# Optimization experiments

Hardware: AMD Instinct MI355X
Metric: run time of the kernel (lower is better)

Reference implementation:

```python
import jax, jax.numpy as jnp
import numpy as np

IN_FEATURES = 4096
OUT_FEATURES = 11008
GROUP_SIZE = 128


def setup_inputs() -> dict:
    key = jax.random.key(0)
    k_x, k_w, k_s, k_z, k_b = jax.random.split(key, 5)
    x = jax.random.normal(k_x, (8, IN_FEATURES), dtype=jnp.float32)
    # packed INT4 weights: two 4-bit values per byte, stored in int32 (0..255)
    weight_q = jax.random.randint(k_w, (OUT_FEATURES, IN_FEATURES // 2), 0, 256, dtype=jnp.int32)
    num_groups = IN_FEATURES // GROUP_SIZE  # 32
    scales = jax.random.uniform(k_s, (OUT_FEATURES, num_groups), dtype=jnp.float32) * 0.01 + 1e-4
    zeros = jax.random.normal(k_z, (OUT_FEATURES, num_groups), dtype=jnp.float32) * 0.05
    bias = jax.random.normal(k_b, (OUT_FEATURES,), dtype=jnp.float32) * 0.02
    return {"x": x, "weight_q": weight_q, "scales": scales, "zeros": zeros, "bias": bias}


def _dequantize(weight_q, scales, zeros):
    # unpack INT4: low nibble first, then high nibble (matches torch stack order)
    low = weight_q & 15
    high = (weight_q >> 4) & 15
    q = jnp.stack([low, high], axis=-1).reshape(OUT_FEATURES, -1)  # [out, in]
    q = q.astype(scales.dtype)
    num_groups = scales.shape[1]
    q = q[:, : num_groups * GROUP_SIZE].reshape(OUT_FEATURES, num_groups, GROUP_SIZE)
    w = q * scales[:, :, None] + zeros[:, :, None]
    return w.reshape(OUT_FEATURES, -1)[:, :IN_FEATURES]


def reference(x, weight_q, scales, zeros, bias):
    w = _dequantize(weight_q, scales, zeros)            # [out, in]
    return x.astype(w.dtype) @ w.T + bias               # [B, out]
```

## Files before the change

### kernel.cpp

```cpp
#include <hip/hip_runtime.h>

typedef _Float16 f16;
typedef __attribute__((ext_vector_type(2))) _Float16 f16x2;
typedef __attribute__((ext_vector_type(4))) _Float16 f16x4;
typedef __attribute__((ext_vector_type(8))) _Float16 f16x8;
typedef __attribute__((ext_vector_type(4))) float f32x4;
typedef __attribute__((ext_vector_type(4))) unsigned u32x4;

constexpr int IN_F  = 4096;
constexpr int OUT_F = 11008;
constexpr int NGRP  = 32;
constexpr int NTILE = OUT_F / 16;
constexpr int PLANE = OUT_F * 8;

__device__ __forceinline__ unsigned dq2(unsigned q, f16x2 sp, f16x2 zp) {
    unsigned t = (((q << 12) | q) & 0x000F000Fu) | 0x64006400u;
    f16x2 u = __builtin_bit_cast(f16x2, t);
    u = u - (f16x2){(_Float16)1024.0f, (_Float16)1024.0f};
    u = u * sp + zp;
    return __builtin_bit_cast(unsigned, u);
}

__device__ __forceinline__ f16x2 bcast(float v) {
    _Float16 h = (_Float16)v;
    return (f16x2){h, h};
}

__global__ void xprep_kernel(const float* __restrict__ x, f16* __restrict__ xh) {
    int i = (blockIdx.x * blockDim.x + threadIdx.x) * 4;
    float4 v = *(const float4*)(x + i);
    f16x4 r = {(f16)v.x, (f16)v.y, (f16)v.z, (f16)v.w};
    *(f16x4*)(xh + i) = r;
}

__global__ __launch_bounds__(256, 4)
void qlin_pipe(const int* __restrict__ wq,
               const float* __restrict__ scales,
               const float* __restrict__ zeros,
               const f16* __restrict__ xh,
               float* __restrict__ wsf)
{
    __shared__ unsigned char wlds[4][2][2048];

    const int tid  = threadIdx.x;
    const int wv   = tid >> 6;
    const int lane = tid & 63;
    const int col  = lane & 15;
    const int kg   = lane >> 4;
    const int bid  = blockIdx.x;
    const int kq   = bid & 3;
    const int ot   = bid >> 2;
    const int o0   = ot * 16;
    const int orow = o0 + col;
    const int k0   = kq * 1024 + wv * 256;
    const int g0   = k0 >> 7;
    const bool mvalid = (col < 8);

    float2 sg = *(const float2*)(scales + (size_t)orow * NGRP + g0);
    float2 zg = *(const float2*)(zeros  + (size_t)orow * NGRP + g0);

    f16x8 af[4][2];
    const f16* xcol = xh + (size_t)col * IN_F + k0 + kg * 8;
    #pragma unroll
    for (int ss = 0; ss < 4; ++ss) {
        if (mvalid) {
            af[ss][0] = *(const f16x8*)(xcol + ss * 64);
            af[ss][1] = *(const f16x8*)(xcol + ss * 64 + 32);
        } else {
            af[ss][0] = (f16x8){0,0,0,0,0,0,0,0};
            af[ss][1] = (f16x8){0,0,0,0,0,0,0,0};
        }
    }

    const char* wb   = (const char*)wq;
    const int   coff = (lane & 7) * 16;

    auto stageW = [&](int ss) {
        const int b = ss & 1;
        #pragma unroll
        for (int j = 0; j < 2; ++j) {
            const int r = j * 8 + (lane >> 3);
            const char* src = wb + (size_t)(o0 + r) * 8192
                              + (size_t)(k0 + ss * 64) * 2
                              + (coff ^ ((r & 7) << 4));
            __builtin_amdgcn_global_load_lds(
                (const __attribute__((address_space(1))) void*)src,
                (__attribute__((address_space(3))) void*)&wlds[wv][b][j * 1024],
                16, 0, 0);
        }
    };

    stageW(0); __builtin_amdgcn_sched_barrier(0);
    stageW(1); __builtin_amdgcn_sched_barrier(0);

    const unsigned rswz = (unsigned)((col & 7) << 4);
    f32x4 acc = {0.f, 0.f, 0.f, 0.f};

    #pragma unroll
    for (int ss = 0; ss < 4; ++ss) {
        if (ss < 3) asm volatile("s_waitcnt vmcnt(2)" ::: "memory");
        else        asm volatile("s_waitcnt vmcnt(0)" ::: "memory");
        __builtin_amdgcn_sched_barrier(0);

        const unsigned char* buf = &wlds[wv][ss & 1][0];
        const int4 qa = *(const int4*)(buf + (col * 128 + ((     kg * 16) ^ rswz)));
        const int4 qb = *(const int4*)(buf + (col * 128 + ((64 + kg * 16) ^ rswz)));

        asm volatile("s_waitcnt lgkmcnt(0)" ::: "memory");
        __builtin_amdgcn_sched_barrier(0);
        if (ss < 2) { stageW(ss + 2); __builtin_amdgcn_sched_barrier(0); }

        const f16x2 s2 = bcast((ss < 2) ? sg.x : sg.y);
        const f16x2 z2 = bcast((ss < 2) ? zg.x : zg.y);
        u32x4 ba = {dq2((unsigned)qa.x, s2, z2), dq2((unsigned)qa.y, s2, z2),
                    dq2((unsigned)qa.z, s2, z2), dq2((unsigned)qa.w, s2, z2)};
        u32x4 bb = {dq2((unsigned)qb.x, s2, z2), dq2((unsigned)qb.y, s2, z2),
                    dq2((unsigned)qb.z, s2, z2), dq2((unsigned)qb.w, s2, z2)};
        acc = __builtin_amdgcn_mfma_f32_16x16x32_f16(af[ss][0],
                __builtin_bit_cast(f16x8, ba), acc, 0, 0, 0);
        acc = __builtin_amdgcn_mfma_f32_16x16x32_f16(af[ss][1],
                __builtin_bit_cast(f16x8, bb), acc, 0, 0, 0);
    }

    *(f32x4*)&wlds[wv][0][lane * 16] = acc;
    __syncthreads();

    if (tid < 32) {
        f32x4 ssum = *(const f32x4*)&wlds[0][0][tid * 16];
        #pragma unroll
        for (int w = 1; w < 4; ++w)
            ssum += *(const f32x4*)&wlds[w][0][tid * 16];
        const int n = tid & 15;
        const int mbase = (tid >> 4) * 4;
        float* plane = wsf + (size_t)kq * PLANE;
        #pragma unroll
        for (int i = 0; i < 4; ++i)
            plane[(size_t)(mbase + i) * OUT_F + o0 + n] = ssum[i];
    }
}

__global__ __launch_bounds__(256)
void reduce_kernel(const float* __restrict__ wsf,
                   const float* __restrict__ bias,
                   float* __restrict__ out)
{
    const int idx = blockIdx.x * 256 + threadIdx.x;
    const int o = idx % OUT_F;
    out[idx] = bias[o] + wsf[idx] + wsf[PLANE + idx]
             + wsf[2 * PLANE + idx] + wsf[3 * PLANE + idx];
}

__global__ __launch_bounds__(256, 4)
void qlin_kernel(const int* __restrict__ wq,
                 const float* __restrict__ scales,
                 const float* __restrict__ zeros,
                 const float* __restrict__ bias,
                 const float* __restrict__ xf,
                 float* __restrict__ out)
{
    __shared__ unsigned char wlds[2][16][1024];
    __shared__ f32x4 red[4][64];

    const int tid  = threadIdx.x;
    const int wv   = tid >> 6;
    const int lane = tid & 63;
    const int col  = lane & 15;
    const int kg   = lane >> 4;
    const int o0   = blockIdx.x * 16;
    const int orow = o0 + col;
    const bool mvalid = (col < 8);

    f16x2 sp[8], zp[8];
    #pragma unroll
    for (int s = 0; s < 8; ++s) {
        sp[s] = bcast(scales[(size_t)orow * NGRP + s * 4 + wv]);
        zp[s] = bcast(zeros [(size_t)orow * NGRP + s * 4 + wv]);
    }

    const char* wtile = (const char*)wq + (size_t)o0 * 8192;
    auto stage = [&](int sl, int bufi) {
        #pragma unroll
        for (int c = 0; c < 4; ++c) {
            const int r = 4 * wv + c;
            const char* src = wtile + (size_t)r * 8192 + sl * 1024
                              + ((lane * 16) ^ ((r & 7) << 4));
            __builtin_amdgcn_global_load_lds(
                (const __attribute__((address_space(1))) void*)src,
                (__attribute__((address_space(3))) void*)&wlds[bufi][r][0],
                16, 0, 0);
        }
    };

    stage(0, 0);
    stage(1, 1);

    const float* xfcol = xf + (size_t)col * IN_F;
    const unsigned swz = (unsigned)((col & 7) << 4);
    f32x4 acc = {0.f, 0.f, 0.f, 0.f};

    #pragma unroll
    for (int s = 0; s < 8; ++s) {
        asm volatile("s_waitcnt vmcnt(0)" ::: "memory");
        __builtin_amdgcn_s_barrier();
        asm volatile("" ::: "memory");

        const f16x2 s2 = sp[s], z2 = zp[s];
        #pragma unroll
        for (int t = 0; t < 4; ++t) {
            const int k = s * 512 + wv * 128 + t * 32 + kg * 8;
            f16x8 af = (f16x8){0,0,0,0,0,0,0,0};
            if (mvalid) {
                float4 a0 = *(const float4*)(xfcol + k);
                float4 a1 = *(const float4*)(xfcol + k + 4);
                af = (f16x8){(f16)a0.x,(f16)a0.y,(f16)a0.z,(f16)a0.w,
                             (f16)a1.x,(f16)a1.y,(f16)a1.z,(f16)a1.w};
            }
            const unsigned off = ((unsigned)(wv * 256 + t * 64 + kg * 16)) ^ swz;
            const int4 q = *(const int4*)&wlds[s & 1][col][off];
            u32x4 bw = {dq2((unsigned)q.x, s2, z2),
                        dq2((unsigned)q.y, s2, z2),
                        dq2((unsigned)q.z, s2, z2),
                        dq2((unsigned)q.w, s2, z2)};
            f16x8 bfr = __builtin_bit_cast(f16x8, bw);
            acc = __builtin_amdgcn_mfma_f32_16x16x32_f16(af, bfr, acc, 0, 0, 0);
        }

        asm volatile("" ::: "memory");
        __builtin_amdgcn_s_barrier();
        if (s < 6) stage(s + 2, s & 1);
    }

    red[wv][lane] = acc;
    __syncthreads();

    if (tid < 64) {
        f32x4 ssum = red[0][tid];
        #pragma unroll
        for (int w = 1; w < 4; ++w) ssum += red[w][tid];
        const int n = tid & 15;
        const float bb = bias[o0 + n];
        const int mbase = (tid >> 4) * 4;
        if (mbase < 8) {
            #pragma unroll
            for (int i = 0; i < 4; ++i)
                out[(size_t)(mbase + i) * OUT_F + o0 + n] = ssum[i] + bb;
        }
    }
}

extern "C" void kernel_launch(void* const* d_in, const int* in_sizes, int n_in,
                              void* d_out, int out_size, void* d_ws, size_t ws_size,
                              hipStream_t stream) {
    const float* x  = (const float*)d_in[0];
    const int*   wq = (const int*)d_in[1];
    const float* sc = (const float*)d_in[2];
    const float* zr = (const float*)d_in[3];
    const float* bs = (const float*)d_in[4];
    float* out = (float*)d_out;
    (void)in_sizes; (void)n_in;

    const size_t planes_b = (size_t)4 * PLANE * sizeof(float);
    const size_t xh_b     = (size_t)8 * IN_F * sizeof(f16);

    if (ws_size >= planes_b + xh_b) {
        float* wsf = (float*)d_ws;
        f16*   xh  = (f16*)((char*)d_ws + planes_b);
        xprep_kernel<<<(8 * IN_F) / (256 * 4), 256, 0, stream>>>(x, xh);
        qlin_pipe<<<NTILE * 4, 256, 0, stream>>>(wq, sc, zr, xh, wsf);
        reduce_kernel<<<PLANE / 256, 256, 0, stream>>>(wsf, bs, out);
    } else {
        qlin_kernel<<<NTILE, 256, 0, stream>>>(wq, sc, zr, bs, x, out);
    }
}
```

Measured before the change: 28.80 us.

## Issue all weight LDS loads up front and zero-pad x to sixteen rows

The double-buffered two-stage weight pipeline becomes a single burst: all four 2KB stages per wave are issued into a larger 8KB-per-wave LDS buffer, with staged vmcnt waits as each stage is consumed. The activation prep kernel now writes a zero-padded 16-row fp16 copy of x, so the main kernel loads A fragments unconditionally and interleaves them with the weight loads. This removes the mid-loop LDS waits and the reissue of stages, and drops the per-lane validity branch. In exchange LDS use per block grows from 16KB to 32KB, which can cap resident blocks per CU, and the prep kernel writes twice as much.

```diff
diff --git a/kernel.cpp b/kernel.cpp
--- a/kernel.cpp
+++ b/kernel.cpp
@@ -26,21 +26,29 @@
     return (f16x2){h, h};
 }
 
-__global__ void xprep_kernel(const float* __restrict__ x, f16* __restrict__ xh) {
-    int i = (blockIdx.x * blockDim.x + threadIdx.x) * 4;
-    float4 v = *(const float4*)(x + i);
-    f16x4 r = {(f16)v.x, (f16)v.y, (f16)v.z, (f16)v.w};
-    *(f16x4*)(xh + i) = r;
+__global__ void xprep16_kernel(const float* __restrict__ x, f16* __restrict__ xh) {
+    const int i4  = blockIdx.x * blockDim.x + threadIdx.x;
+    const int k4  = i4 * 4;
+    const int row = k4 >> 12;
+    const int kk  = k4 & 4095;
+    f16x4 r;
+    if (row < 8) {
+        float4 v = *(const float4*)(x + (size_t)row * IN_F + kk);
+        r = (f16x4){(f16)v.x, (f16)v.y, (f16)v.z, (f16)v.w};
+    } else {
+        r = (f16x4){0, 0, 0, 0};
+    }
+    *(f16x4*)(xh + (size_t)row * IN_F + kk) = r;
 }
 
 __global__ __launch_bounds__(256, 4)
-void qlin_pipe(const int* __restrict__ wq,
-               const float* __restrict__ scales,
-               const float* __restrict__ zeros,
-               const f16* __restrict__ xh,
-               float* __restrict__ wsf)
+void qlin_burst(const int* __restrict__ wq,
+                const float* __restrict__ scales,
+                const float* __restrict__ zeros,
+                const f16* __restrict__ xh,
+                float* __restrict__ wsf)
 {
-    __shared__ unsigned char wlds[4][2][2048];
+    __shared__ unsigned char wlds[4][8192];
 
     const int tid  = threadIdx.x;
     const int wv   = tid >> 6;
@@ -54,29 +62,19 @@
     const int orow = o0 + col;
     const int k0   = kq * 1024 + wv * 256;
     const int g0   = k0 >> 7;
-    const bool mvalid = (col < 8);
 
     float2 sg = *(const float2*)(scales + (size_t)orow * NGRP + g0);
     float2 zg = *(const float2*)(zeros  + (size_t)orow * NGRP + g0);
-
-    f16x8 af[4][2];
-    const f16* xcol = xh + (size_t)col * IN_F + k0 + kg * 8;
-    #pragma unroll
-    for (int ss = 0; ss < 4; ++ss) {
-        if (mvalid) {
-            af[ss][0] = *(const f16x8*)(xcol + ss * 64);
-            af[ss][1] = *(const f16x8*)(xcol + ss * 64 + 32);
-        } else {
-            af[ss][0] = (f16x8){0,0,0,0,0,0,0,0};
-            af[ss][1] = (f16x8){0,0,0,0,0,0,0,0};
-        }
-    }
+    __builtin_amdgcn_sched_barrier(0);
 
     const char* wb   = (const char*)wq;
     const int   coff = (lane & 7) * 16;
-
-    auto stageW = [&](int ss) {
-        const int b = ss & 1;
+    const f16*  xcol = xh + (size_t)col * IN_F + k0 + kg * 8;
+
+    f16x8 af[4][2];
+
+    #pragma unroll
+    for (int ss = 0; ss < 4; ++ss) {
         #pragma unroll
         for (int j = 0; j < 2; ++j) {
             const int r = j * 8 + (lane >> 3);
@@ -85,30 +83,30 @@
                               + (coff ^ ((r & 7) << 4));
             __builtin_amdgcn_global_load_lds(
                 (const __attribute__((address_space(1))) void*)src,
-                (__attribute__((address_space(3))) void*)&wlds[wv][b][j * 1024],
+                (__attribute__((address_space(3))) void*)&wlds[wv][ss * 2048 + j * 1024],
                 16, 0, 0);
         }
-    };
-
-    stageW(0); __builtin_amdgcn_sched_barrier(0);
-    stageW(1); __builtin_amdgcn_sched_barrier(0);
-
-    const unsigned rswz = (unsigned)((col & 7) << 4);
+        af[ss][0] = *(const f16x8*)(xcol + ss * 64);
+        af[ss][1] = *(const f16x8*)(xcol + ss * 64 + 32);
+        __builtin_amdgcn_sched_barrier(0);
+    }
+
+    const unsigned rswz  = (unsigned)((col & 7) << 4);
+    const unsigned rbase = (unsigned)((col >> 3) * 1024 + (col & 7) * 128);
+
     f32x4 acc = {0.f, 0.f, 0.f, 0.f};
 
     #pragma unroll
     for (int ss = 0; ss < 4; ++ss) {
-        if (ss < 3) asm volatile("s_waitcnt vmcnt(2)" ::: "memory");
-        else        asm volatile("s_waitcnt vmcnt(0)" ::: "memory");
+        if      (ss == 0) asm volatile("s_waitcnt vmcnt(12)" ::: "memory");
+        else if (ss == 1) asm volatile("s_waitcnt vmcnt(8)"  ::: "memory");
+        else if (ss == 2) asm volatile("s_waitcnt vmcnt(4)"  ::: "memory");
+        else              asm volatile("s_waitcnt vmcnt(0)"  ::: "memory");
         __builtin_amdgcn_sched_barrier(0);
 
-        const unsigned char* buf = &wlds[wv][ss & 1][0];
-        const int4 qa = *(const int4*)(buf + (col * 128 + ((     kg * 16) ^ rswz)));
-        const int4 qb = *(const int4*)(buf + (col * 128 + ((64 + kg * 16) ^ rswz)));
-
-        asm volatile("s_waitcnt lgkmcnt(0)" ::: "memory");
-        __builtin_amdgcn_sched_barrier(0);
-        if (ss < 2) { stageW(ss + 2); __builtin_amdgcn_sched_barrier(0); }
+        const unsigned char* buf = &wlds[wv][ss * 2048];
+        const int4 qa = *(const int4*)(buf + rbase + ((     kg * 16) ^ rswz));
+        const int4 qb = *(const int4*)(buf + rbase + ((64 + kg * 16) ^ rswz));
 
         const f16x2 s2 = bcast((ss < 2) ? sg.x : sg.y);
         const f16x2 z2 = bcast((ss < 2) ? zg.x : zg.y);
@@ -122,14 +120,14 @@
                 __builtin_bit_cast(f16x8, bb), acc, 0, 0, 0);
     }
 
-    *(f32x4*)&wlds[wv][0][lane * 16] = acc;
+    *(f32x4*)&wlds[wv][lane * 16] = acc;
     __syncthreads();
 
     if (tid < 32) {
-        f32x4 ssum = *(const f32x4*)&wlds[0][0][tid * 16];
+        f32x4 ssum = *(const f32x4*)&wlds[0][tid * 16];
         #pragma unroll
         for (int w = 1; w < 4; ++w)
-            ssum += *(const f32x4*)&wlds[w][0][tid * 16];
+            ssum += *(const f32x4*)&wlds[w][tid * 16];
         const int n = tid & 15;
         const int mbase = (tid >> 4) * 4;
         float* plane = wsf + (size_t)kq * PLANE;
@@ -260,13 +258,13 @@
     (void)in_sizes; (void)n_in;
 
     const size_t planes_b = (size_t)4 * PLANE * sizeof(float);
-    const size_t xh_b     = (size_t)8 * IN_F * sizeof(f16);
+    const size_t xh_b     = (size_t)16 * IN_F * sizeof(f16);
 
     if (ws_size >= planes_b + xh_b) {
         float* wsf = (float*)d_ws;
         f16*   xh  = (f16*)((char*)d_ws + planes_b);
-        xprep_kernel<<<(8 * IN_F) / (256 * 4), 256, 0, stream>>>(x, xh);
-        qlin_pipe<<<NTILE * 4, 256, 0, stream>>>(wq, sc, zr, xh, wsf);
+        xprep16_kernel<<<(16 * IN_F) / (256 * 4), 256, 0, stream>>>(x, xh);
+        qlin_burst<<<NTILE * 4, 256, 0, stream>>>(wq, sc, zr, xh, wsf);
         reduce_kernel<<<PLANE / 256, 256, 0, stream>>>(wsf, bs, out);
     } else {
         qlin_kernel<<<NTILE, 256, 0, stream>>>(wq, sc, zr, bs, x, out);
```

Measured after the change: 29.01 us. Within noise of the previous version (+0.7%).
